# Kernel optimization log

Measured on AMD Instinct MI355X. Metric: run time of the kernel, lower is better.

Reference implementation:

```python
import jax, jax.numpy as jnp
import numpy as np

B, S, D, H = 4, 2048, 512, 8
DEPTH = D // H


def setup_inputs() -> dict:
    key = jax.random.key(0)
    ks = jax.random.split(key, 12)
    s = 0.02
    return {
        "q": jax.random.normal(ks[0], (B, S, D), jnp.float32),
        "k": jax.random.normal(ks[1], (B, S, D), jnp.float32),
        "v": jax.random.normal(ks[2], (B, S, D), jnp.float32),
        "mask": jax.random.randint(ks[3], (B, 1, 1, S), 0, 2, jnp.int32),
        "wq": jax.random.normal(ks[4], (D, D), jnp.float32) * s,
        "bq": jnp.zeros((D,), jnp.float32),
        "wk": jax.random.normal(ks[5], (D, D), jnp.float32) * s,
        "bk": jnp.zeros((D,), jnp.float32),
        "wv": jax.random.normal(ks[6], (D, D), jnp.float32) * s,
        "bv": jnp.zeros((D,), jnp.float32),
        "wo": jax.random.normal(ks[7], (D, D), jnp.float32) * s,
        "bo": jnp.zeros((D,), jnp.float32),
    }


def _split_heads(x):
    # [B,S,D] -> [B,H,S,depth]
    b = x.shape[0]
    return x.reshape(b, -1, H, DEPTH).transpose(0, 2, 1, 3)


def reference(q, k, v, mask, wq, bq, wk, bk, wv, bv, wo, bo):
    qh = _split_heads(q @ wq + bq)
    kh = _split_heads(k @ wk + bk)
    vh = _split_heads(v @ wv + bv)
    scale = 1.0 / jnp.sqrt(jnp.float32(DEPTH))
    logits = jnp.einsum("bhqd,bhkd->bhqk", qh, kh) * scale
    logits = logits + mask.astype(jnp.float32) * -1e9
    attn = jax.nn.softmax(logits, axis=-1)  # [B,H,Sq,Sk]
    out = jnp.einsum("bhqk,bhkd->bhqd", attn, vh)
    out = out.transpose(0, 2, 1, 3).reshape(q.shape[0], -1, D)
    out = out @ wo + bo
    return out, attn
```

## Files before the change

### kernel.cpp

```cpp
#include <hip/hip_runtime.h>

#define B_ 4
#define S_ 2048
#define D_ 512
#define H_ 8
#define DP_ 64
#define NT_ (S_/64)

typedef __attribute__((ext_vector_type(4))) float f32x4;
typedef __attribute__((ext_vector_type(8))) short short8;

__device__ __forceinline__ short f2bf(float f){
  unsigned u = __float_as_uint(f);
  u += 0x7fff + ((u >> 16) & 1);
  return (short)(u >> 16);
}

#define SWZ(r, kb) ((r)*64 + ((kb) ^ (((r)&7)<<3)))

#define WAITV(N) do{ asm volatile("s_waitcnt vmcnt(" #N ")" ::: "memory"); }while(0)
#define BAR() do{ __builtin_amdgcn_s_barrier(); __builtin_amdgcn_sched_barrier(0); }while(0)

template<int NC>
__device__ __forceinline__ void stage_swz(const short* __restrict__ g, int rowStride,
                                          short* shbase, int w, int l){
  #pragma unroll
  for(int i = 0; i < NC; ++i){
    int byte = (w*NC + i)*1024 + l*16;
    int row = byte >> 7;
    int gs = ((byte >> 4) & 7) ^ (row & 7);
    const short* src = g + (size_t)row*rowStride + gs*8;
    __builtin_amdgcn_global_load_lds((const __attribute__((address_space(1))) void*)src,
        (__attribute__((address_space(3))) void*)(shbase + (w*NC + i)*512), 16, 0, 0);
  }
}

__global__ void k_prep(const float* __restrict__ w0, const float* __restrict__ w1,
                       const float* __restrict__ w2, const float* __restrict__ w3,
                       short* __restrict__ t0, short* __restrict__ t1,
                       short* __restrict__ t2, short* __restrict__ t3){
  __shared__ float t[32][33];
  const float* w = blockIdx.z == 0 ? w0 : blockIdx.z == 1 ? w1 : blockIdx.z == 2 ? w2 : w3;
  short* wt = blockIdx.z == 0 ? t0 : blockIdx.z == 1 ? t1 : blockIdx.z == 2 ? t2 : t3;
  int bx = blockIdx.x * 32, by = blockIdx.y * 32;
  int tx = threadIdx.x, ty = threadIdx.y;
  #pragma unroll
  for(int i = 0; i < 32; i += 8) t[ty + i][tx] = w[(by + ty + i) * D_ + bx + tx];
  __syncthreads();
  #pragma unroll
  for(int i = 0; i < 32; i += 8) wt[(bx + ty + i) * D_ + by + tx] = f2bf(t[tx][ty + i]);
}

__global__ void k_cast(const float* __restrict__ q, const float* __restrict__ k,
                       const float* __restrict__ v, const int* __restrict__ mask,
                       short* __restrict__ dst, float* __restrict__ mb){
  if(blockIdx.z == 3){
    int i = blockIdx.x * 256 + threadIdx.x;
    if(i < B_ * S_) mb[i] = mask[i] ? -1.0e9f : 0.0f;
    return;
  }
  const float* s = blockIdx.z == 0 ? q : blockIdx.z == 1 ? k : v;
  short* d = dst + (size_t)blockIdx.z * (B_ * S_ * D_);
  int i = blockIdx.x * 256 + threadIdx.x;
  float4 a = ((const float4*)s)[i * 2];
  float4 b = ((const float4*)s)[i * 2 + 1];
  short8 o;
  o[0]=f2bf(a.x); o[1]=f2bf(a.y); o[2]=f2bf(a.z); o[3]=f2bf(a.w);
  o[4]=f2bf(b.x); o[5]=f2bf(b.y); o[6]=f2bf(b.z); o[7]=f2bf(b.w);
  ((short8*)d)[i] = o;
}

__global__ __launch_bounds__(256) void k_gemm_qkv(const short* __restrict__ Xall,
        const short* __restrict__ WTall, const float* __restrict__ b0,
        const float* __restrict__ b1, const float* __restrict__ b2,
        short* __restrict__ qh, short* __restrict__ kh, short* __restrict__ vvt){
  __shared__ __align__(16) short As[8192];
  __shared__ __align__(16) short Bs[8192];
  const int z = blockIdx.z;
  const short* X  = Xall + (size_t)z * (B_*S_*D_);
  const short* WT = WTall + (size_t)z * (D_*D_);
  const float* bias = z==0 ? b0 : (z==1 ? b1 : b2);
  const int t = threadIdx.x, l = t & 63, w = t >> 6;
  const int lr = l & 15, lg = l >> 4;
  const int m0 = blockIdx.x * 128, n0 = blockIdx.y * 128;
  const int wr = w >> 1, wc = w & 1;
  const short* Xb = X + (size_t)m0 * D_;
  const short* Wb = WT + (size_t)n0 * D_;
  f32x4 acc[4][4] = {};
  for(int kt = 0; kt < D_ / 64; ++kt){
    stage_swz<4>(Xb + kt*64, D_, As, w, l);
    stage_swz<4>(Wb + kt*64, D_, Bs, w, l);
    __syncthreads();
    #pragma unroll
    for(int ks = 0; ks < 2; ++ks){
      const int kb = ks*32 + lg*8;
      short8 a[4], b[4];
      #pragma unroll
      for(int mt = 0; mt < 4; ++mt)
        a[mt] = *reinterpret_cast<const short8*>(&As[SWZ(wr*64 + mt*16 + lr, kb)]);
      #pragma unroll
      for(int nt = 0; nt < 4; ++nt)
        b[nt] = *reinterpret_cast<const short8*>(&Bs[SWZ(wc*64 + nt*16 + lr, kb)]);
      __builtin_amdgcn_s_setprio(1);
      #pragma unroll
      for(int mt = 0; mt < 4; ++mt)
        #pragma unroll
        for(int nt = 0; nt < 4; ++nt)
          acc[mt][nt] = __builtin_amdgcn_mfma_f32_16x16x32_bf16(a[mt], b[nt], acc[mt][nt], 0, 0, 0);
      __builtin_amdgcn_s_setprio(0);
    }
    __syncthreads();
  }
  #pragma unroll
  for(int mt = 0; mt < 4; ++mt){
    #pragma unroll
    for(int nt = 0; nt < 4; ++nt){
      const int n = n0 + wc*64 + nt*16 + lr;
      const int m4 = m0 + wr*64 + mt*16 + lg*4;
      float vals[4];
      #pragma unroll
      for(int r = 0; r < 4; ++r) vals[r] = acc[mt][nt][r] + bias[n];
      if(z == 2){
        short4 pv4;
        pv4.x = f2bf(vals[0]); pv4.y = f2bf(vals[1]); pv4.z = f2bf(vals[2]); pv4.w = f2bf(vals[3]);
        *reinterpret_cast<short4*>(&vvt[
            (((size_t)((m4 >> 11) * H_ + (n >> 6))) * DP_ + (n & 63)) * S_ + (m4 & 2047)]) = pv4;
      } else {
        short* dst = z == 0 ? qh : kh;
        #pragma unroll
        for(int r = 0; r < 4; ++r){
          int m = m4 + r;
          dst[(((size_t)((m >> 11) * H_ + (n >> 6))) * S_ + (m & 2047)) * DP_ + (n & 63)] = f2bf(vals[r]);
        }
      }
    }
  }
}

__global__ __launch_bounds__(256) void k_gemm_out(const short* __restrict__ X,
        const short* __restrict__ WT, const float* __restrict__ bias,
        float* __restrict__ Out){
  __shared__ __align__(16) short As[8192];
  __shared__ __align__(16) short Bs[8192];
  const int t = threadIdx.x, l = t & 63, w = t >> 6;
  const int lr = l & 15, lg = l >> 4;
  const int m0 = blockIdx.x * 128, n0 = blockIdx.y * 128;
  const int wr = w >> 1, wc = w & 1;
  const short* Xb = X + (size_t)m0 * D_;
  const short* Wb = WT + (size_t)n0 * D_;
  f32x4 acc[4][4] = {};
  for(int kt = 0; kt < D_ / 64; ++kt){
    stage_swz<4>(Xb + kt*64, D_, As, w, l);
    stage_swz<4>(Wb + kt*64, D_, Bs, w, l);
    __syncthreads();
    #pragma unroll
    for(int ks = 0; ks < 2; ++ks){
      const int kb = ks*32 + lg*8;
      short8 a[4], b[4];
      #pragma unroll
      for(int mt = 0; mt < 4; ++mt)
        a[mt] = *reinterpret_cast<const short8*>(&As[SWZ(wr*64 + mt*16 + lr, kb)]);
      #pragma unroll
      for(int nt = 0; nt < 4; ++nt)
        b[nt] = *reinterpret_cast<const short8*>(&Bs[SWZ(wc*64 + nt*16 + lr, kb)]);
      __builtin_amdgcn_s_setprio(1);
      #pragma unroll
      for(int mt = 0; mt < 4; ++mt)
        #pragma unroll
        for(int nt = 0; nt < 4; ++nt)
          acc[mt][nt] = __builtin_amdgcn_mfma_f32_16x16x32_bf16(a[mt], b[nt], acc[mt][nt], 0, 0, 0);
      __builtin_amdgcn_s_setprio(0);
    }
    __syncthreads();
  }
  #pragma unroll
  for(int mt = 0; mt < 4; ++mt){
    #pragma unroll
    for(int nt = 0; nt < 4; ++nt){
      const int n = n0 + wc*64 + nt*16 + lr;
      const int m4 = m0 + wr*64 + mt*16 + lg*4;
      #pragma unroll
      for(int r = 0; r < 4; ++r)
        Out[(size_t)(m4 + r) * D_ + n] = acc[mt][nt][r] + bias[n];
    }
  }
}

__global__ __launch_bounds__(512, 4) void k_attn(const short* __restrict__ qh,
                                                 const short* __restrict__ kh,
                                                 const short* __restrict__ vt,
                                                 const float* __restrict__ mb,
                                                 float* __restrict__ attn,
                                                 short* __restrict__ ctx){
  __shared__ __align__(16) short Sh[28672];
  const int t = threadIdx.x, l = t & 63, w = t >> 6;
  const int lr = l & 15, lg = l >> 4;
  int lin = blockIdx.y * 16 + blockIdx.x;
  int sw = (lin & 7) * 64 + (lin >> 3);
  const int bh = sw >> 4, b = bh >> 3, h = bh & 7;
  const int q0 = (sw & 15) * 128;
  const short* Qb = qh + (size_t)bh * S_ * DP_ + (size_t)q0 * DP_;
  const short* Kb = kh + (size_t)bh * S_ * DP_;
  const short* Vtb = vt + (size_t)bh * DP_ * S_;
  const float* Mbb = mb + b * S_;
  float* Mlds = (float*)(Sh + 24576);
  const float scale = 0.125f;

  stage_swz<2>(Qb, DP_, Sh + 16384, w, l);
  __builtin_amdgcn_global_load_lds(
      (const __attribute__((address_space(1))) void*)(Mbb + w*256 + l*4),
      (__attribute__((address_space(3))) void*)(Mlds + w*256 + l*4), 16, 0, 0);
  stage_swz<1>(Kb, DP_, Sh, w, l);
  stage_swz<1>(Kb + 4096, DP_, Sh + 4096, w, l);
  WAITV(2); BAR();
  short8 bq0, bq1;
  {
    int r = w * 16 + lr;
    bq0 = *reinterpret_cast<const short8*>(&Sh[16384 + SWZ(r, lg * 8)]);
    bq1 = *reinterpret_cast<const short8*>(&Sh[16384 + SWZ(r, 32 + lg * 8)]);
  }

  float ps = 0.f;
  for(int kt = 0; kt < NT_; ++kt){
    if(kt < NT_ - 1){ WAITV(1); } else { WAITV(0); }
    BAR();
    if(kt + 2 < NT_)
      stage_swz<1>(Kb + (size_t)(kt + 2) * 4096, DP_, Sh + ((kt + 2) % 3) * 4096, w, l);
    const short* Kc = Sh + (kt % 3) * 4096;
    const float* Ml = Mlds + kt * 64;
    #pragma unroll
    for(int st = 0; st < 4; ++st){
      const float4 mv = ((const float4*)Ml)[st * 4 + lg];
      short8 ak0 = *reinterpret_cast<const short8*>(&Kc[SWZ(st * 16 + lr, lg * 8)]);
      short8 ak1 = *reinterpret_cast<const short8*>(&Kc[SWZ(st * 16 + lr, 32 + lg * 8)]);
      __builtin_amdgcn_s_setprio(1);
      f32x4 c = {};
      c = __builtin_amdgcn_mfma_f32_16x16x32_bf16(ak0, bq0, c, 0, 0, 0);
      c = __builtin_amdgcn_mfma_f32_16x16x32_bf16(ak1, bq1, c, 0, 0, 0);
      __builtin_amdgcn_s_setprio(0);
      ps += __expf(__builtin_fmaf(c[0], scale, mv.x));
      ps += __expf(__builtin_fmaf(c[1], scale, mv.y));
      ps += __expf(__builtin_fmaf(c[2], scale, mv.z));
      ps += __expf(__builtin_fmaf(c[3], scale, mv.w));
    }
  }
  stage_swz<1>(Kb, DP_, Sh, w, l);
  stage_swz<1>(Vtb, S_, Sh + 8192, w, l);
  ps += __shfl_xor(ps, 16, 64);
  ps += __shfl_xor(ps, 32, 64);
  const float rinv = 1.f / ps;

  f32x4 o[4] = {};
  short* Pw = Sh + 16384 + w * 1024;
  for(int kt = 0; kt < NT_; ++kt){
    if(kt == 0){ WAITV(0); } else { WAITV(4); }
    BAR();
    if(kt + 1 < NT_){
      stage_swz<1>(Kb + (size_t)(kt + 1) * 4096, DP_, Sh + ((kt + 1) & 1) * 4096, w, l);
      stage_swz<1>(Vtb + (size_t)(kt + 1) * 64, S_, Sh + 8192 + ((kt + 1) & 1) * 4096, w, l);
    }
    const short* Kc = Sh + (kt & 1) * 4096;
    const short* Vc = Sh + 8192 + (kt & 1) * 4096;
    const float* Ml = Mlds + kt * 64;
    #pragma unroll
    for(int st = 0; st < 4; ++st){
      const float4 mv = ((const float4*)Ml)[st * 4 + lg];
      short8 ak0 = *reinterpret_cast<const short8*>(&Kc[SWZ(st * 16 + lr, lg * 8)]);
      short8 ak1 = *reinterpret_cast<const short8*>(&Kc[SWZ(st * 16 + lr, 32 + lg * 8)]);
      __builtin_amdgcn_s_setprio(1);
      f32x4 c = {};
      c = __builtin_amdgcn_mfma_f32_16x16x32_bf16(ak0, bq0, c, 0, 0, 0);
      c = __builtin_amdgcn_mfma_f32_16x16x32_bf16(ak1, bq1, c, 0, 0, 0);
      __builtin_amdgcn_s_setprio(0);
      float4 pw;
      pw.x = __expf(__builtin_fmaf(c[0], scale, mv.x)) * rinv;
      pw.y = __expf(__builtin_fmaf(c[1], scale, mv.y)) * rinv;
      pw.z = __expf(__builtin_fmaf(c[2], scale, mv.z)) * rinv;
      pw.w = __expf(__builtin_fmaf(c[3], scale, mv.w)) * rinv;
      const int q = q0 + w * 16 + lr;
      *reinterpret_cast<float4*>(&attn[((size_t)bh * S_ + q) * S_ + kt * 64 + st * 16 + lg * 4]) = pw;
      short4 pb;
      pb.x = f2bf(pw.x); pb.y = f2bf(pw.y); pb.z = f2bf(pw.z); pb.w = f2bf(pw.w);
      *reinterpret_cast<short4*>(&Pw[SWZ(lr, st * 16 + lg * 4)]) = pb;
    }
    #pragma unroll
    for(int ks = 0; ks < 2; ++ks){
      short8 pa = *reinterpret_cast<const short8*>(&Pw[SWZ(lr, ks * 32 + lg * 8)]);
      __builtin_amdgcn_s_setprio(1);
      #pragma unroll
      for(int dt = 0; dt < 4; ++dt){
        short8 vb = *reinterpret_cast<const short8*>(&Vc[SWZ(dt * 16 + lr, ks * 32 + lg * 8)]);
        o[dt] = __builtin_amdgcn_mfma_f32_16x16x32_bf16(pa, vb, o[dt], 0, 0, 0);
      }
      __builtin_amdgcn_s_setprio(0);
    }
  }
  #pragma unroll
  for(int dt = 0; dt < 4; ++dt){
    #pragma unroll
    for(int r = 0; r < 4; ++r){
      int q = q0 + w * 16 + lg * 4 + r;
      int dd = h * 64 + dt * 16 + lr;
      ctx[((size_t)b * S_ + q) * D_ + dd] = f2bf(o[dt][r]);
    }
  }
}

extern "C" void kernel_launch(void* const* d_in, const int* in_sizes, int n_in,
                              void* d_out, int out_size, void* d_ws, size_t ws_size,
                              hipStream_t stream){
  const float* q  = (const float*)d_in[0];
  const float* k  = (const float*)d_in[1];
  const float* v  = (const float*)d_in[2];
  const int* mask = (const int*)d_in[3];
  const float* wq = (const float*)d_in[4];
  const float* bq = (const float*)d_in[5];
  const float* wk = (const float*)d_in[6];
  const float* bk = (const float*)d_in[7];
  const float* wv = (const float*)d_in[8];
  const float* bv = (const float*)d_in[9];
  const float* wo = (const float*)d_in[10];
  const float* bo = (const float*)d_in[11];

  float* out  = (float*)d_out;
  float* attn = out + (size_t)B_ * S_ * D_;

  char* ws = (char*)d_ws;
  short* qkvc = (short*)ws;
  short* qh  = (short*)(ws + 25165824);
  short* kh  = (short*)(ws + 33554432);
  short* vvt = (short*)(ws + 41943040);
  short* ctx = (short*)(ws + 50331648);
  short* wT  = (short*)(ws + 58720256);
  float* mb  = (float*)(ws + 58720256 + 4 * 524288);

  hipLaunchKernelGGL(k_prep, dim3(16, 16, 4), dim3(32, 8), 0, stream,
                     wq, wk, wv, wo, wT, wT + 262144, wT + 2 * 262144, wT + 3 * 262144);
  hipLaunchKernelGGL(k_cast, dim3(2048, 1, 4), dim3(256), 0, stream, q, k, v, mask, qkvc, mb);

  hipLaunchKernelGGL(k_gemm_qkv, dim3(64, 4, 3), dim3(256), 0, stream,
                     qkvc, wT, bq, bk, bv, qh, kh, vvt);

  hipLaunchKernelGGL(k_attn, dim3(16, 32), dim3(512), 0, stream, qh, kh, vvt, mb, attn, ctx);

  hipLaunchKernelGGL(k_gemm_out, dim3(64, 4), dim3(256), 0, stream, ctx, wT + 3 * 262144, bo, out);
}
```

Baseline: 252.5 us.

## Keep softmax probabilities in registers for PV MFMA and merge prep kernels

The attention kernel now permutes which K rows each lane computes so the QK^T MFMA output lands directly in the A-operand layout of the PV MFMA. The probabilities are packed to bf16 with v_cvt_pk_bf16_f32 instead of going through an LDS round trip, and a new swizzle (SWZ2) is adapted to the new row access pattern. Separately, the weight-transpose and input-cast kernels are merged into one launch to save a kernel launch. The permuted row mapping changes the attn store pattern, which may affect write coalescing.

```diff
diff --git a/kernel.cpp b/kernel.cpp
--- a/kernel.cpp
+++ b/kernel.cpp
@@ -9,6 +9,7 @@
 
 typedef __attribute__((ext_vector_type(4))) float f32x4;
 typedef __attribute__((ext_vector_type(8))) short short8;
+typedef __attribute__((ext_vector_type(4))) int i32x4;
 
 __device__ __forceinline__ short f2bf(float f){
   unsigned u = __float_as_uint(f);
@@ -16,7 +17,15 @@
   return (short)(u >> 16);
 }
 
+__device__ __forceinline__ int cvtpk(float lo, float hi){
+  int r;
+  asm("v_cvt_pk_bf16_f32 %0, %1, %2" : "=v"(r) : "v"(lo), "v"(hi));
+  return r;
+}
+
 #define SWZ(r, kb) ((r)*64 + ((kb) ^ (((r)&7)<<3)))
+#define F2(r) ((((r)&3)) | ((((r)>>3)&1)<<2))
+#define SWZ2(r, kb) ((r)*64 + ((kb) ^ (F2(r)<<3)))
 
 #define WAITV(N) do{ asm volatile("s_waitcnt vmcnt(" #N ")" ::: "memory"); }while(0)
 #define BAR() do{ __builtin_amdgcn_s_barrier(); __builtin_amdgcn_sched_barrier(0); }while(0)
@@ -34,40 +43,56 @@
         (__attribute__((address_space(3))) void*)(shbase + (w*NC + i)*512), 16, 0, 0);
   }
 }
-
-__global__ void k_prep(const float* __restrict__ w0, const float* __restrict__ w1,
-                       const float* __restrict__ w2, const float* __restrict__ w3,
-                       short* __restrict__ t0, short* __restrict__ t1,
-                       short* __restrict__ t2, short* __restrict__ t3){
-  __shared__ float t[32][33];
-  const float* w = blockIdx.z == 0 ? w0 : blockIdx.z == 1 ? w1 : blockIdx.z == 2 ? w2 : w3;
-  short* wt = blockIdx.z == 0 ? t0 : blockIdx.z == 1 ? t1 : blockIdx.z == 2 ? t2 : t3;
-  int bx = blockIdx.x * 32, by = blockIdx.y * 32;
-  int tx = threadIdx.x, ty = threadIdx.y;
-  #pragma unroll
-  for(int i = 0; i < 32; i += 8) t[ty + i][tx] = w[(by + ty + i) * D_ + bx + tx];
-  __syncthreads();
-  #pragma unroll
-  for(int i = 0; i < 32; i += 8) wt[(bx + ty + i) * D_ + by + tx] = f2bf(t[tx][ty + i]);
-}
-
-__global__ void k_cast(const float* __restrict__ q, const float* __restrict__ k,
-                       const float* __restrict__ v, const int* __restrict__ mask,
-                       short* __restrict__ dst, float* __restrict__ mb){
-  if(blockIdx.z == 3){
-    int i = blockIdx.x * 256 + threadIdx.x;
-    if(i < B_ * S_) mb[i] = mask[i] ? -1.0e9f : 0.0f;
-    return;
-  }
-  const float* s = blockIdx.z == 0 ? q : blockIdx.z == 1 ? k : v;
-  short* d = dst + (size_t)blockIdx.z * (B_ * S_ * D_);
-  int i = blockIdx.x * 256 + threadIdx.x;
-  float4 a = ((const float4*)s)[i * 2];
-  float4 b = ((const float4*)s)[i * 2 + 1];
-  short8 o;
-  o[0]=f2bf(a.x); o[1]=f2bf(a.y); o[2]=f2bf(a.z); o[3]=f2bf(a.w);
-  o[4]=f2bf(b.x); o[5]=f2bf(b.y); o[6]=f2bf(b.z); o[7]=f2bf(b.w);
-  ((short8*)d)[i] = o;
+template<int NC>
+__device__ __forceinline__ void stage_swz2(const short* __restrict__ g, int rowStride,
+                                           short* shbase, int w, int l){
+  #pragma unroll
+  for(int i = 0; i < NC; ++i){
+    int byte = (w*NC + i)*1024 + l*16;
+    int row = byte >> 7;
+    int gs = ((byte >> 4) & 7) ^ F2(row);
+    const short* src = g + (size_t)row*rowStride + gs*8;
+    __builtin_amdgcn_global_load_lds((const __attribute__((address_space(1))) void*)src,
+        (__attribute__((address_space(3))) void*)(shbase + (w*NC + i)*512), 16, 0, 0);
+  }
+}
+
+__global__ __launch_bounds__(256) void k_pre(const float* __restrict__ q,
+        const float* __restrict__ k, const float* __restrict__ v,
+        const int* __restrict__ mask,
+        const float* __restrict__ w0, const float* __restrict__ w1,
+        const float* __restrict__ w2, const float* __restrict__ w3,
+        short* __restrict__ wT, short* __restrict__ qkvc, float* __restrict__ mb){
+  __shared__ float tt[32][33];
+  const int bi = blockIdx.x, t = threadIdx.x;
+  if(bi < 1024){
+    const int z = bi >> 8;
+    const float* w = z == 0 ? w0 : z == 1 ? w1 : z == 2 ? w2 : w3;
+    short* wt = wT + z * 262144;
+    const int bxy = bi & 255;
+    const int bx = (bxy & 15) * 32, by = (bxy >> 4) * 32;
+    const int tx = t & 31, ty = t >> 5;
+    #pragma unroll
+    for(int i = 0; i < 32; i += 8) tt[ty + i][tx] = w[(by + ty + i) * D_ + bx + tx];
+    __syncthreads();
+    #pragma unroll
+    for(int i = 0; i < 32; i += 8) wt[(bx + ty + i) * D_ + by + tx] = f2bf(tt[tx][ty + i]);
+  } else if(bi < 7168){
+    const int ci = bi - 1024;
+    const int z = ci >> 11;
+    const float* s = z == 0 ? q : z == 1 ? k : v;
+    short* d = qkvc + (size_t)z * (B_ * S_ * D_);
+    int i = (ci & 2047) * 256 + t;
+    float4 a = ((const float4*)s)[i * 2];
+    float4 b = ((const float4*)s)[i * 2 + 1];
+    short8 o;
+    o[0]=f2bf(a.x); o[1]=f2bf(a.y); o[2]=f2bf(a.z); o[3]=f2bf(a.w);
+    o[4]=f2bf(b.x); o[5]=f2bf(b.y); o[6]=f2bf(b.z); o[7]=f2bf(b.w);
+    ((short8*)d)[i] = o;
+  } else {
+    int i = (bi - 7168) * 256 + t;
+    mb[i] = mask[i] ? -1.0e9f : 0.0f;
+  }
 }
 
 __global__ __launch_bounds__(256) void k_gemm_qkv(const short* __restrict__ Xall,
@@ -206,18 +231,18 @@
   float* Mlds = (float*)(Sh + 24576);
   const float scale = 0.125f;
 
-  stage_swz<2>(Qb, DP_, Sh + 16384, w, l);
+  stage_swz2<2>(Qb, DP_, Sh + 16384, w, l);
   __builtin_amdgcn_global_load_lds(
       (const __attribute__((address_space(1))) void*)(Mbb + w*256 + l*4),
       (__attribute__((address_space(3))) void*)(Mlds + w*256 + l*4), 16, 0, 0);
-  stage_swz<1>(Kb, DP_, Sh, w, l);
-  stage_swz<1>(Kb + 4096, DP_, Sh + 4096, w, l);
+  stage_swz2<1>(Kb, DP_, Sh, w, l);
+  stage_swz2<1>(Kb + 4096, DP_, Sh + 4096, w, l);
   WAITV(2); BAR();
   short8 bq0, bq1;
   {
     int r = w * 16 + lr;
-    bq0 = *reinterpret_cast<const short8*>(&Sh[16384 + SWZ(r, lg * 8)]);
-    bq1 = *reinterpret_cast<const short8*>(&Sh[16384 + SWZ(r, 32 + lg * 8)]);
+    bq0 = *reinterpret_cast<const short8*>(&Sh[16384 + SWZ2(r, lg * 8)]);
+    bq1 = *reinterpret_cast<const short8*>(&Sh[16384 + SWZ2(r, 32 + lg * 8)]);
   }
 
   float ps = 0.f;
@@ -225,14 +250,14 @@
     if(kt < NT_ - 1){ WAITV(1); } else { WAITV(0); }
     BAR();
     if(kt + 2 < NT_)
-      stage_swz<1>(Kb + (size_t)(kt + 2) * 4096, DP_, Sh + ((kt + 2) % 3) * 4096, w, l);
+      stage_swz2<1>(Kb + (size_t)(kt + 2) * 4096, DP_, Sh + ((kt + 2) % 3) * 4096, w, l);
     const short* Kc = Sh + (kt % 3) * 4096;
     const float* Ml = Mlds + kt * 64;
     #pragma unroll
     for(int st = 0; st < 4; ++st){
-      const float4 mv = ((const float4*)Ml)[st * 4 + lg];
-      short8 ak0 = *reinterpret_cast<const short8*>(&Kc[SWZ(st * 16 + lr, lg * 8)]);
-      short8 ak1 = *reinterpret_cast<const short8*>(&Kc[SWZ(st * 16 + lr, 32 + lg * 8)]);
+      const float4 mv = *(const float4*)&Ml[st * 16 + lg * 4];
+      short8 ak0 = *reinterpret_cast<const short8*>(&Kc[SWZ2(st * 16 + lr, lg * 8)]);
+      short8 ak1 = *reinterpret_cast<const short8*>(&Kc[SWZ2(st * 16 + lr, 32 + lg * 8)]);
       __builtin_amdgcn_s_setprio(1);
       f32x4 c = {};
       c = __builtin_amdgcn_mfma_f32_16x16x32_bf16(ak0, bq0, c, 0, 0, 0);
@@ -244,29 +269,34 @@
       ps += __expf(__builtin_fmaf(c[3], scale, mv.w));
     }
   }
-  stage_swz<1>(Kb, DP_, Sh, w, l);
-  stage_swz<1>(Vtb, S_, Sh + 8192, w, l);
+  stage_swz2<1>(Kb, DP_, Sh, w, l);
+  stage_swz2<1>(Vtb, S_, Sh + 8192, w, l);
   ps += __shfl_xor(ps, 16, 64);
   ps += __shfl_xor(ps, 32, 64);
   const float rinv = 1.f / ps;
 
   f32x4 o[4] = {};
-  short* Pw = Sh + 16384 + w * 1024;
+  const int grow = ((lr >> 2) << 3) + (lr & 3);
   for(int kt = 0; kt < NT_; ++kt){
     if(kt == 0){ WAITV(0); } else { WAITV(4); }
     BAR();
     if(kt + 1 < NT_){
-      stage_swz<1>(Kb + (size_t)(kt + 1) * 4096, DP_, Sh + ((kt + 1) & 1) * 4096, w, l);
-      stage_swz<1>(Vtb + (size_t)(kt + 1) * 64, S_, Sh + 8192 + ((kt + 1) & 1) * 4096, w, l);
+      stage_swz2<1>(Kb + (size_t)(kt + 1) * 4096, DP_, Sh + ((kt + 1) & 1) * 4096, w, l);
+      stage_swz2<1>(Vtb + (size_t)(kt + 1) * 64, S_, Sh + 8192 + ((kt + 1) & 1) * 4096, w, l);
     }
     const short* Kc = Sh + (kt & 1) * 4096;
     const short* Vc = Sh + 8192 + (kt & 1) * 4096;
     const float* Ml = Mlds + kt * 64;
+    const int q = q0 + w * 16 + lr;
+    i32x4 pav[2];
     #pragma unroll
     for(int st = 0; st < 4; ++st){
-      const float4 mv = ((const float4*)Ml)[st * 4 + lg];
-      short8 ak0 = *reinterpret_cast<const short8*>(&Kc[SWZ(st * 16 + lr, lg * 8)]);
-      short8 ak1 = *reinterpret_cast<const short8*>(&Kc[SWZ(st * 16 + lr, 32 + lg * 8)]);
+      const int ks = st >> 1, h4 = st & 1;
+      const int row = grow + h4 * 4 + ks * 32;
+      const int mcol = ks * 32 + h4 * 4 + lg * 8;
+      const float4 mv = *(const float4*)&Ml[mcol];
+      short8 ak0 = *reinterpret_cast<const short8*>(&Kc[SWZ2(row, lg * 8)]);
+      short8 ak1 = *reinterpret_cast<const short8*>(&Kc[SWZ2(row, 32 + lg * 8)]);
       __builtin_amdgcn_s_setprio(1);
       f32x4 c = {};
       c = __builtin_amdgcn_mfma_f32_16x16x32_bf16(ak0, bq0, c, 0, 0, 0);
@@ -277,19 +307,17 @@
       pw.y = __expf(__builtin_fmaf(c[1], scale, mv.y)) * rinv;
       pw.z = __expf(__builtin_fmaf(c[2], scale, mv.z)) * rinv;
       pw.w = __expf(__builtin_fmaf(c[3], scale, mv.w)) * rinv;
-      const int q = q0 + w * 16 + lr;
-      *reinterpret_cast<float4*>(&attn[((size_t)bh * S_ + q) * S_ + kt * 64 + st * 16 + lg * 4]) = pw;
-      short4 pb;
-      pb.x = f2bf(pw.x); pb.y = f2bf(pw.y); pb.z = f2bf(pw.z); pb.w = f2bf(pw.w);
-      *reinterpret_cast<short4*>(&Pw[SWZ(lr, st * 16 + lg * 4)]) = pb;
+      *reinterpret_cast<float4*>(&attn[((size_t)bh * S_ + q) * S_ + kt * 64 + mcol]) = pw;
+      pav[ks][h4 * 2 + 0] = cvtpk(pw.x, pw.y);
+      pav[ks][h4 * 2 + 1] = cvtpk(pw.z, pw.w);
     }
     #pragma unroll
     for(int ks = 0; ks < 2; ++ks){
-      short8 pa = *reinterpret_cast<const short8*>(&Pw[SWZ(lr, ks * 32 + lg * 8)]);
+      short8 pa = __builtin_bit_cast(short8, pav[ks]);
       __builtin_amdgcn_s_setprio(1);
       #pragma unroll
       for(int dt = 0; dt < 4; ++dt){
-        short8 vb = *reinterpret_cast<const short8*>(&Vc[SWZ(dt * 16 + lr, ks * 32 + lg * 8)]);
+        short8 vb = *reinterpret_cast<const short8*>(&Vc[SWZ2(dt * 16 + lr, ks * 32 + lg * 8)]);
         o[dt] = __builtin_amdgcn_mfma_f32_16x16x32_bf16(pa, vb, o[dt], 0, 0, 0);
       }
       __builtin_amdgcn_s_setprio(0);
@@ -334,9 +362,8 @@
   short* wT  = (short*)(ws + 58720256);
   float* mb  = (float*)(ws + 58720256 + 4 * 524288);
 
-  hipLaunchKernelGGL(k_prep, dim3(16, 16, 4), dim3(32, 8), 0, stream,
-                     wq, wk, wv, wo, wT, wT + 262144, wT + 2 * 262144, wT + 3 * 262144);
-  hipLaunchKernelGGL(k_cast, dim3(2048, 1, 4), dim3(256), 0, stream, q, k, v, mask, qkvc, mb);
+  hipLaunchKernelGGL(k_pre, dim3(7200), dim3(256), 0, stream,
+                     q, k, v, mask, wq, wk, wv, wo, wT, qkvc, mb);
 
   hipLaunchKernelGGL(k_gemm_qkv, dim3(64, 4, 3), dim3(256), 0, stream,
                      qkvc, wT, bq, bk, bv, qh, kh, vvt);
```

Result: no change. 250.8 us (-0.7%).
